# Kernel optimization log

Measured on AMD Instinct MI355X. Metric: run time of the kernel, lower is better.

Reference implementation:

```python
import jax, jax.numpy as jnp
import numpy as np
import math

D = 512          # model_dim
H = 8            # num_heads
HD = D // H      # head_dim
L = 6            # num_layers
FF = 2 * D       # dim_feedforward
IN_DIM = 24
MAX_LEN = 1024   # positional_embedding_dim (sinusoidal max_len)
NUM_CLASSES = 1
B, S = 8, 1024
EPS = 1e-5


def make_sinusoidal_pe(max_len, d_model):
    position = np.arange(max_len, dtype=np.float32)[:, None]
    div_term = np.exp(np.arange(0, d_model, 2, dtype=np.float32) * (-math.log(10000.0) / d_model))
    pe = np.zeros((max_len, d_model), dtype=np.float32)
    pe[:, 0::2] = np.sin(position * div_term)
    pe[:, 1::2] = np.cos(position * div_term)
    return jnp.asarray(pe)


def layer_norm(x, g, b):
    mu = jnp.mean(x, axis=-1, keepdims=True)
    var = jnp.mean(jnp.square(x - mu), axis=-1, keepdims=True)
    return (x - mu) * jax.lax.rsqrt(var + EPS) * g + b


def setup_inputs() -> dict:
    key = jax.random.key(0)
    ks = jax.random.split(key, 16)
    xavier = lambda k, shape: jax.random.uniform(
        k, shape, jnp.float32,
        -math.sqrt(6.0 / (shape[-2] + shape[-1])),
        math.sqrt(6.0 / (shape[-2] + shape[-1])))
    inp = {
        'x': jax.random.normal(ks[0], (B, S, IN_DIM), jnp.float32),
        'positions': jax.random.randint(ks[1], (B, S), 0, MAX_LEN),
        'pe': make_sinusoidal_pe(MAX_LEN, D),
        'input_W': xavier(ks[2], (IN_DIM, D)),
        'input_b': jnp.zeros((D,), jnp.float32),
        'qkv_W': xavier(ks[3], (L, D, 3 * D)),
        'qkv_b': jnp.zeros((L, 3 * D), jnp.float32),
        'o_W': xavier(ks[4], (L, D, D)),
        'o_b': jnp.zeros((L, D), jnp.float32),
        'ff1_W': xavier(ks[5], (L, D, FF)),
        'ff1_b': jnp.zeros((L, FF), jnp.float32),
        'ff2_W': xavier(ks[6], (L, FF, D)),
        'ff2_b': jnp.zeros((L, D), jnp.float32),
        'ln1_g': jnp.ones((L, D), jnp.float32),
        'ln1_b': jnp.zeros((L, D), jnp.float32),
        'ln2_g': jnp.ones((L, D), jnp.float32),
        'ln2_b': jnp.zeros((L, D), jnp.float32),
        'out1_W': xavier(ks[7], (D, D)),
        'out1_b': jnp.zeros((D,), jnp.float32),
        'outln_g': jnp.ones((D,), jnp.float32),
        'outln_b': jnp.zeros((D,), jnp.float32),
        'out2_W': xavier(ks[8], (D, NUM_CLASSES)),
        'out2_b': jnp.zeros((NUM_CLASSES,), jnp.float32),
    }
    return inp


def reference(x, positions, pe, input_W, input_b, qkv_W, qkv_b, o_W, o_b,
              ff1_W, ff1_b, ff2_W, ff2_b, ln1_g, ln1_b, ln2_g, ln2_b,
              out1_W, out1_b, outln_g, outln_b, out2_W, out2_b):
    b, s, _ = x.shape
    # input projection + sinusoidal positional encoding gathered at positions
    h = x @ input_W + input_b + pe[positions]            # [B,S,D]
    scale = 1.0 / math.sqrt(HD)
    for l in range(qkv_W.shape[0]):
        qkv = (h @ qkv_W[l] + qkv_b[l]).reshape(b, s, H, 3 * HD)
        q = jnp.transpose(qkv[..., :HD], (0, 2, 1, 3))           # [B,H,S,hd]
        k = jnp.transpose(qkv[..., HD:2 * HD], (0, 2, 1, 3))
        v = jnp.transpose(qkv[..., 2 * HD:], (0, 2, 1, 3))
        logits = jnp.einsum('bhqd,bhkd->bhqk', q, k) * scale     # [B,H,S,S]
        attn = jax.nn.softmax(logits, axis=-1)
        vals = jnp.einsum('bhqk,bhkd->bhqd', attn, v)
        vals = jnp.transpose(vals, (0, 2, 1, 3)).reshape(b, s, D)
        attn_out = vals @ o_W[l] + o_b[l]
        h = layer_norm(h + attn_out, ln1_g[l], ln1_b[l])
        ff = jax.nn.relu(h @ ff1_W[l] + ff1_b[l]) @ ff2_W[l] + ff2_b[l]
        h = layer_norm(h + ff, ln2_g[l], ln2_b[l])
    pooled = jnp.mean(h, axis=1)                                 # [B,D] mean pooling
    o = jax.nn.relu(layer_norm(pooled @ out1_W + out1_b, outln_g, outln_b))
    return o @ out2_W + out2_b                                   # [B,num_classes]
```

## Files before the change

kernel.cpp:

```cpp
#include <hip/hip_runtime.h>
#include <cstddef>

#define EPS 1e-5f

typedef short bf16x8 __attribute__((ext_vector_type(8)));
typedef float f32x4 __attribute__((ext_vector_type(4)));
typedef unsigned short u16x8 __attribute__((ext_vector_type(8)));
typedef unsigned short u16x4 __attribute__((ext_vector_type(4)));

__device__ __forceinline__ unsigned short f2bf(float x) {
  unsigned u = __float_as_uint(x);
  return (unsigned short)((u + 0x7FFFu + ((u >> 16) & 1u)) >> 16);
}

__device__ __forceinline__ void gl2lds16(const unsigned short* g, unsigned short* l) {
  __builtin_amdgcn_global_load_lds(
      (const __attribute__((address_space(1))) unsigned int*)g,
      (__attribute__((address_space(3))) unsigned int*)l, 16, 0, 0);
}

__global__ __launch_bounds__(512) void inproj_kernel(
    const float* __restrict__ x, const int* __restrict__ pos,
    const float* __restrict__ pe, const float* __restrict__ Wp,
    const float* __restrict__ bp, float* __restrict__ h,
    unsigned short* __restrict__ hb) {
  int t = blockIdx.x, d = threadIdx.x;
  __shared__ float xs[24];
  if (d < 24) xs[d] = x[(size_t)t * 24 + d];
  __syncthreads();
  float acc = bp[d] + pe[(size_t)pos[t] * 512 + d];
#pragma unroll
  for (int k = 0; k < 24; ++k) acc += xs[k] * Wp[k * 512 + d];
  h[(size_t)t * 512 + d] = acc;
  hb[(size_t)t * 512 + d] = f2bf(acc);
}

__global__ __launch_bounds__(256) void wcast_kernel(
    const float* __restrict__ qw, const float* __restrict__ ow,
    const float* __restrict__ f1w, const float* __restrict__ f2w,
    unsigned short* __restrict__ qd, unsigned short* __restrict__ od,
    unsigned short* __restrict__ f1d, unsigned short* __restrict__ f2d) {
  __shared__ float sm[64][65];
  int bid = blockIdx.x;
  const float* src; unsigned short* dst; int K, N, tile;
  if (bid < 192)      { src = qw;  dst = qd;  K = 512;  N = 1536; tile = bid; }
  else if (bid < 256) { src = ow;  dst = od;  K = 512;  N = 512;  tile = bid - 192; }
  else if (bid < 384) { src = f1w; dst = f1d; K = 512;  N = 1024; tile = bid - 256; }
  else                { src = f2w; dst = f2d; K = 1024; N = 512;  tile = bid - 384; }
  int nt = N >> 6;
  int tk = tile / nt, tn = tile % nt;
  int k0 = tk * 64, n0 = tn * 64;
  int tid = threadIdx.x;
#pragma unroll
  for (int it = 0; it < 16; ++it) {
    int idx = it * 256 + tid;
    int ki = idx >> 6, ni = idx & 63;
    sm[ki][ni] = src[(size_t)(k0 + ki) * N + n0 + ni];
  }
  __syncthreads();
#pragma unroll
  for (int it = 0; it < 16; ++it) {
    int idx = it * 256 + tid;
    int ni = idx >> 6, ki = idx & 63;
    dst[(size_t)(n0 + ni) * K + k0 + ki] = f2bf(sm[ki][ni]);
  }
}

template <int MODE>
__global__ __launch_bounds__(256) void gemm_bf16(
    const unsigned short* __restrict__ A, const unsigned short* __restrict__ Bw,
    const float* __restrict__ bias, float* __restrict__ Cf,
    unsigned short* __restrict__ Cb, unsigned short* __restrict__ q_out,
    unsigned short* __restrict__ k_out, unsigned short* __restrict__ v_out,
    int M, int N, int K) {
  __shared__ unsigned short As[128 * 32];
  __shared__ unsigned short Bs[128 * 32];
  int tid = threadIdx.x;
  int w = tid >> 6, l = tid & 63;
  int wm = w >> 1, wn = w & 1;
  int cl = l & 15, kg = l >> 4;
  int n0 = blockIdx.x * 128, m0 = blockIdx.y * 128;
  f32x4 acc[4][4];
#pragma unroll
  for (int i = 0; i < 4; ++i)
#pragma unroll
    for (int j = 0; j < 4; ++j) acc[i][j] = f32x4{0.f, 0.f, 0.f, 0.f};

  const unsigned short* Ap = A + (size_t)m0 * K;
  const unsigned short* Bp = Bw + (size_t)n0 * K;

  for (int k0 = 0; k0 < K; k0 += 32) {
    __syncthreads();
#pragma unroll
    for (int c = 0; c < 2; ++c) {
      int idx = c * 256 + tid;
      int r = idx >> 2, kq = idx & 3;
      gl2lds16(Ap + (size_t)r * K + k0 + kq * 8, &As[(c * 256 + w * 64) * 8]);
      gl2lds16(Bp + (size_t)r * K + k0 + kq * 8, &Bs[(c * 256 + w * 64) * 8]);
    }
    __syncthreads();
    bf16x8 af[4], bfr[4];
#pragma unroll
    for (int i = 0; i < 4; ++i) {
      af[i]  = *(const bf16x8*)&As[(wm * 64 + i * 16 + cl) * 32 + kg * 8];
      bfr[i] = *(const bf16x8*)&Bs[(wn * 64 + i * 16 + cl) * 32 + kg * 8];
    }
#pragma unroll
    for (int i = 0; i < 4; ++i)
#pragma unroll
      for (int j = 0; j < 4; ++j)
        acc[i][j] = __builtin_amdgcn_mfma_f32_16x16x32_bf16(af[i], bfr[j], acc[i][j], 0, 0, 0);
  }

  int rl = kg * 4;
#pragma unroll
  for (int i = 0; i < 4; ++i) {
    int mbase = m0 + wm * 64 + i * 16 + rl;
#pragma unroll
    for (int j = 0; j < 4; ++j) {
      int col = n0 + wn * 64 + j * 16 + cl;
      float bv = bias[col];
      if (MODE == 0) {
#pragma unroll
        for (int r = 0; r < 4; ++r)
          Cf[(size_t)(mbase + r) * N + col] = acc[i][j][r] + bv;
      } else if (MODE == 1) {
#pragma unroll
        for (int r = 0; r < 4; ++r)
          Cb[(size_t)(mbase + r) * N + col] = f2bf(fmaxf(acc[i][j][r] + bv, 0.f));
      } else {
        int hh = col / 192;
        int rem = col - hh * 192;
        int which = rem >> 6, d = rem & 63;
        int b = mbase >> 10, s = mbase & 1023;
        if (which == 2) {
          u16x4 pk;
#pragma unroll
          for (int r = 0; r < 4; ++r) pk[r] = f2bf(acc[i][j][r] + bv);
          *(u16x4*)&v_out[((size_t)((b * 8 + hh) * 64 + d)) * 1024 + s] = pk;
        } else {
          unsigned short* dst = (which == 0) ? q_out : k_out;
#pragma unroll
          for (int r = 0; r < 4; ++r)
            dst[(((size_t)(b * 8 + hh)) * 1024 + s + r) * 64 + d] = f2bf(acc[i][j][r] + bv);
        }
      }
    }
  }
}

__global__ __launch_bounds__(512) void attn_mfma(
    const unsigned short* __restrict__ qT, const unsigned short* __restrict__ kT,
    const unsigned short* __restrict__ vT, unsigned short* __restrict__ valsb) {
  __shared__ unsigned short Ks[2][64 * 64];
  __shared__ unsigned short Vs[2][64 * 64];
  __shared__ unsigned short Ps[8][16 * 64];

  int bh = blockIdx.x >> 3;
  int qt = blockIdx.x & 7;
  int b = bh >> 3, h = bh & 7;
  int tid = threadIdx.x;
  int w = tid >> 6, l = tid & 63;
  int cl = l & 15, kg = l >> 4, rl = kg * 4;

  const unsigned short* kgb = kT + (size_t)bh * 65536;
  const unsigned short* vgb = vT + (size_t)bh * 65536;

  int q0 = qt * 128 + w * 16;
  const unsigned short* qbase = qT + ((size_t)bh * 1024 + q0) * 64;
  bf16x8 aq[2];
  aq[0] = *(const bf16x8*)(qbase + cl * 64 + kg * 8);
  aq[1] = *(const bf16x8*)(qbase + cl * 64 + 32 + kg * 8);

  int sk = tid >> 3, sa = tid & 7;
  int kboff = (sk * 128 + sa * 16) ^ ((sk & 7) << 4);

  const float C = 0.125f * 1.44269504f;

  float m2[4], lsum[4];
  f32x4 accO[4];
#pragma unroll
  for (int r = 0; r < 4; ++r) { m2[r] = -1e30f; lsum[r] = 0.f; }
#pragma unroll
  for (int df = 0; df < 4; ++df) accO[df] = f32x4{0.f, 0.f, 0.f, 0.f};

  char* Pw = (char*)&Ps[w][0];

  uint4 kv = *(const uint4*)(kgb + (size_t)sk * 64 + sa * 8);
  uint4 vv = *(const uint4*)(vgb + (size_t)sk * 1024 + sa * 8);
  *(uint4*)((char*)Ks[0] + kboff) = kv;
  *(uint4*)((char*)Vs[0] + kboff) = vv;
  __syncthreads();

  for (int c = 0; c < 16; ++c) {
    int cur = c & 1;
    if (c < 15) {
      kv = *(const uint4*)(kgb + (size_t)(c + 1) * 4096 + sk * 64 + sa * 8);
      vv = *(const uint4*)(vgb + (size_t)sk * 1024 + (c + 1) * 64 + sa * 8);
    }

    f32x4 s[4];
#pragma unroll
    for (int kf = 0; kf < 4; ++kf) {
      s[kf] = f32x4{0.f, 0.f, 0.f, 0.f};
#pragma unroll
      for (int ks = 0; ks < 2; ++ks) {
        int row = kf * 16 + cl;
        int boff = (row * 128 + ks * 64 + kg * 16) ^ ((row & 7) << 4);
        bf16x8 bk = *(const bf16x8*)((char*)Ks[cur] + boff);
        s[kf] = __builtin_amdgcn_mfma_f32_16x16x32_bf16(aq[ks], bk, s[kf], 0, 0, 0);
      }
    }

    float cm[4];
#pragma unroll
    for (int r = 0; r < 4; ++r)
      cm[r] = fmaxf(fmaxf(s[0][r], s[1][r]), fmaxf(s[2][r], s[3][r]));
#pragma unroll
    for (int off = 1; off < 16; off <<= 1)
#pragma unroll
      for (int r = 0; r < 4; ++r) cm[r] = fmaxf(cm[r], __shfl_xor(cm[r], off));

    float alpha[4];
#pragma unroll
    for (int r = 0; r < 4; ++r) {
      float mn = fmaxf(m2[r], cm[r] * C);
      alpha[r] = exp2f(m2[r] - mn);
      m2[r] = mn;
    }

    float rs[4] = {0.f, 0.f, 0.f, 0.f};
#pragma unroll
    for (int kf = 0; kf < 4; ++kf)
#pragma unroll
      for (int r = 0; r < 4; ++r) {
        float p = exp2f(s[kf][r] * C - m2[r]);
        rs[r] += p;
        int row = rl + r;
        int boff = (row * 128 + (kf * 16 + cl) * 2) ^ ((row & 7) << 4);
        *(unsigned short*)(Pw + boff) = f2bf(p);
      }
#pragma unroll
    for (int off = 1; off < 16; off <<= 1)
#pragma unroll
      for (int r = 0; r < 4; ++r) rs[r] += __shfl_xor(rs[r], off);
#pragma unroll
    for (int r = 0; r < 4; ++r) lsum[r] = lsum[r] * alpha[r] + rs[r];
#pragma unroll
    for (int df = 0; df < 4; ++df)
#pragma unroll
      for (int r = 0; r < 4; ++r) accO[df][r] *= alpha[r];

#pragma unroll
    for (int ks = 0; ks < 2; ++ks) {
      int pboff = (cl * 128 + ks * 64 + kg * 16) ^ ((cl & 7) << 4);
      bf16x8 ap = *(const bf16x8*)(Pw + pboff);
#pragma unroll
      for (int df = 0; df < 4; ++df) {
        int d = df * 16 + cl;
        int vboff = (d * 128 + ks * 64 + kg * 16) ^ ((d & 7) << 4);
        bf16x8 bv = *(const bf16x8*)((char*)Vs[cur] + vboff);
        accO[df] = __builtin_amdgcn_mfma_f32_16x16x32_bf16(ap, bv, accO[df], 0, 0, 0);
      }
    }

    if (c < 15) {
      *(uint4*)((char*)Ks[cur ^ 1] + kboff) = kv;
      *(uint4*)((char*)Vs[cur ^ 1] + kboff) = vv;
    }
    __syncthreads();
  }

  float inv[4];
#pragma unroll
  for (int r = 0; r < 4; ++r) inv[r] = 1.f / lsum[r];
#pragma unroll
  for (int df = 0; df < 4; ++df)
#pragma unroll
    for (int r = 0; r < 4; ++r) {
      int q = q0 + rl + r;
      int d = df * 16 + cl;
      valsb[(((size_t)b * 1024) + q) * 512 + h * 64 + d] = f2bf(accO[df][r] * inv[r]);
    }
}

__global__ __launch_bounds__(256) void ln_residual(
    float* __restrict__ h, const float* __restrict__ res,
    const float* __restrict__ g, const float* __restrict__ bb,
    unsigned short* __restrict__ hb) {
  int row = blockIdx.x * 4 + (threadIdx.x >> 6);
  int lane = threadIdx.x & 63;
  size_t base = (size_t)row * 512 + lane * 8;
  float4 v0 = *(const float4*)&h[base];
  float4 v1 = *(const float4*)&h[base + 4];
  float4 r0 = *(const float4*)&res[base];
  float4 r1 = *(const float4*)&res[base + 4];
  float xv[8];
  xv[0] = v0.x + r0.x; xv[1] = v0.y + r0.y; xv[2] = v0.z + r0.z; xv[3] = v0.w + r0.w;
  xv[4] = v1.x + r1.x; xv[5] = v1.y + r1.y; xv[6] = v1.z + r1.z; xv[7] = v1.w + r1.w;
  float s = 0.f, sq = 0.f;
#pragma unroll
  for (int i = 0; i < 8; ++i) { s += xv[i]; sq += xv[i] * xv[i]; }
#pragma unroll
  for (int off = 32; off; off >>= 1) { s += __shfl_xor(s, off); sq += __shfl_xor(sq, off); }
  float mu = s * (1.f / 512.f);
  float var = sq * (1.f / 512.f) - mu * mu;
  float rstd = rsqrtf(var + EPS);
  float4 g0 = *(const float4*)&g[lane * 8];
  float4 g1 = *(const float4*)&g[lane * 8 + 4];
  float4 b0 = *(const float4*)&bb[lane * 8];
  float4 b1 = *(const float4*)&bb[lane * 8 + 4];
  float o[8];
  o[0] = (xv[0] - mu) * rstd * g0.x + b0.x;
  o[1] = (xv[1] - mu) * rstd * g0.y + b0.y;
  o[2] = (xv[2] - mu) * rstd * g0.z + b0.z;
  o[3] = (xv[3] - mu) * rstd * g0.w + b0.w;
  o[4] = (xv[4] - mu) * rstd * g1.x + b1.x;
  o[5] = (xv[5] - mu) * rstd * g1.y + b1.y;
  o[6] = (xv[6] - mu) * rstd * g1.z + b1.z;
  o[7] = (xv[7] - mu) * rstd * g1.w + b1.w;
  *(float4*)&h[base] = make_float4(o[0], o[1], o[2], o[3]);
  *(float4*)&h[base + 4] = make_float4(o[4], o[5], o[6], o[7]);
  u16x8 hv;
#pragma unroll
  for (int i = 0; i < 8; ++i) hv[i] = f2bf(o[i]);
  *(u16x8*)&hb[base] = hv;
}

__global__ __launch_bounds__(512) void pool_kernel(
    const float* __restrict__ h, float* __restrict__ partial) {
  int b = blockIdx.x >> 3, c = blockIdx.x & 7, d = threadIdx.x;
  float s = 0.f;
  for (int t = 0; t < 128; ++t)
    s += h[((size_t)b * 1024 + c * 128 + t) * 512 + d];
  partial[(size_t)blockIdx.x * 512 + d] = s;
}

__global__ __launch_bounds__(512) void head_kernel(
    const float* __restrict__ partial, const float* __restrict__ W1,
    const float* __restrict__ b1, const float* __restrict__ g,
    const float* __restrict__ bb, const float* __restrict__ W2,
    const float* __restrict__ b2, float* __restrict__ out) {
  int b = blockIdx.x, tid = threadIdx.x;
  int wid = tid >> 6, lane = tid & 63;
  __shared__ float ps[512];
  __shared__ float red_s[8];
  __shared__ float red_q[8];
  float pv = 0.f;
#pragma unroll
  for (int c = 0; c < 8; ++c) pv += partial[((size_t)(b * 8 + c)) * 512 + tid];
  ps[tid] = pv * (1.f / 1024.f);
  __syncthreads();
  float acc = b1[tid];
  for (int k = 0; k < 512; ++k) acc += ps[k] * W1[(size_t)k * 512 + tid];
  float s = acc, sq = acc * acc;
#pragma unroll
  for (int off = 32; off; off >>= 1) { s += __shfl_xor(s, off); sq += __shfl_xor(sq, off); }
  if (lane == 0) { red_s[wid] = s; red_q[wid] = sq; }
  __syncthreads();
  float S = 0.f, Q = 0.f;
#pragma unroll
  for (int i = 0; i < 8; ++i) { S += red_s[i]; Q += red_q[i]; }
  float mu = S * (1.f / 512.f);
  float var = Q * (1.f / 512.f) - mu * mu;
  float rstd = rsqrtf(var + EPS);
  float z = (acc - mu) * rstd * g[tid] + bb[tid];
  float r = fmaxf(z, 0.f);
  float v = r * W2[tid];
#pragma unroll
  for (int off = 32; off; off >>= 1) v += __shfl_xor(v, off);
  __syncthreads();
  if (lane == 0) red_s[wid] = v;
  __syncthreads();
  if (tid == 0) {
    float t = 0.f;
#pragma unroll
    for (int i = 0; i < 8; ++i) t += red_s[i];
    out[b] = t + b2[0];
  }
}

extern "C" void kernel_launch(void* const* d_in, const int* in_sizes, int n_in,
                              void* d_out, int out_size, void* d_ws, size_t ws_size,
                              hipStream_t stream) {
  const float* x    = (const float*)d_in[0];
  const int*   pos  = (const int*)d_in[1];
  const float* pe   = (const float*)d_in[2];
  const float* inW  = (const float*)d_in[3];
  const float* inb  = (const float*)d_in[4];
  const float* qkvW = (const float*)d_in[5];
  const float* qkvb = (const float*)d_in[6];
  const float* oW   = (const float*)d_in[7];
  const float* ob   = (const float*)d_in[8];
  const float* f1W  = (const float*)d_in[9];
  const float* f1b  = (const float*)d_in[10];
  const float* f2W  = (const float*)d_in[11];
  const float* f2b  = (const float*)d_in[12];
  const float* l1g  = (const float*)d_in[13];
  const float* l1b  = (const float*)d_in[14];
  const float* l2g  = (const float*)d_in[15];
  const float* l2b  = (const float*)d_in[16];
  const float* o1W  = (const float*)d_in[17];
  const float* o1b  = (const float*)d_in[18];
  const float* og   = (const float*)d_in[19];
  const float* obb  = (const float*)d_in[20];
  const float* o2W  = (const float*)d_in[21];
  const float* o2b  = (const float*)d_in[22];
  float* out = (float*)d_out;

  char* W = (char*)d_ws;
  float*          h     = (float*)(W + 0);
  unsigned short* hb    = (unsigned short*)(W + 16777216);
  unsigned short* qTb   = (unsigned short*)(W + 25165824);
  unsigned short* kTb   = (unsigned short*)(W + 33554432);
  unsigned short* vTb   = (unsigned short*)(W + 41943040);
  unsigned short* valsb = (unsigned short*)(W + 50331648);
  float*          projf = (float*)(W + 25165824);
  unsigned short* ff1b  = (unsigned short*)(W + 41943040);
  unsigned short* wt    = (unsigned short*)(W + 58720256);
  float*          part  = (float*)(W + 62914560);

  unsigned short* wt_qkv = wt;
  unsigned short* wt_o   = wt + 786432;
  unsigned short* wt_f1  = wt + 1048576;
  unsigned short* wt_f2  = wt + 1572864;

  inproj_kernel<<<8192, 512, 0, stream>>>(x, pos, pe, inW, inb, h, hb);

  for (int l = 0; l < 6; ++l) {
    wcast_kernel<<<512, 256, 0, stream>>>(
        qkvW + (size_t)l * 512 * 1536, oW + (size_t)l * 512 * 512,
        f1W + (size_t)l * 512 * 1024, f2W + (size_t)l * 1024 * 512,
        wt_qkv, wt_o, wt_f1, wt_f2);

    gemm_bf16<2><<<dim3(12, 64), 256, 0, stream>>>(
        hb, wt_qkv, qkvb + l * 1536, nullptr, nullptr, qTb, kTb, vTb,
        8192, 1536, 512);

    attn_mfma<<<512, 512, 0, stream>>>(qTb, kTb, vTb, valsb);

    gemm_bf16<0><<<dim3(4, 64), 256, 0, stream>>>(
        valsb, wt_o, ob + l * 512, projf, nullptr, nullptr, nullptr, nullptr,
        8192, 512, 512);

    ln_residual<<<2048, 256, 0, stream>>>(h, projf, l1g + l * 512, l1b + l * 512, hb);

    gemm_bf16<1><<<dim3(8, 64), 256, 0, stream>>>(
        hb, wt_f1, f1b + l * 1024, nullptr, ff1b, nullptr, nullptr, nullptr,
        8192, 1024, 512);

    gemm_bf16<0><<<dim3(4, 64), 256, 0, stream>>>(
        ff1b, wt_f2, f2b + l * 512, projf, nullptr, nullptr, nullptr, nullptr,
        8192, 512, 1024);

    ln_residual<<<2048, 256, 0, stream>>>(h, projf, l2g + l * 512, l2b + l * 512, hb);
  }

  pool_kernel<<<64, 512, 0, stream>>>(h, part);
  head_kernel<<<8, 512, 0, stream>>>(part, o1W, o1b, og, obb, o2W, o2b, out);
}
```

Baseline: 1.221 ms.

## Widen GEMM K-tile with swizzled LDS and restructure attention with lazy rescaling

The GEMM now stages 64-wide K tiles with an XOR-swizzled LDS layout, halving the number of barrier-separated iterations and reducing bank conflicts. The attention kernel processes 128-key chunks in single-buffered LDS with register prefetch. It also skips the online-softmax max update and rescale unless some row's max grows by more than a threshold, and defers the row-sum shuffle reduction to the end. This cuts per-chunk shuffles, exp work and barriers, at the cost of more LDS per block, possible occupancy loss, and the loss of double buffering in attention.

```diff
diff --git a/kernel.cpp b/kernel.cpp
--- a/kernel.cpp
+++ b/kernel.cpp
@@ -73,8 +73,8 @@
     unsigned short* __restrict__ Cb, unsigned short* __restrict__ q_out,
     unsigned short* __restrict__ k_out, unsigned short* __restrict__ v_out,
     int M, int N, int K) {
-  __shared__ unsigned short As[128 * 32];
-  __shared__ unsigned short Bs[128 * 32];
+  __shared__ unsigned short As[128 * 64];
+  __shared__ unsigned short Bs[128 * 64];
   int tid = threadIdx.x;
   int w = tid >> 6, l = tid & 63;
   int wm = w >> 1, wn = w & 1;
@@ -89,27 +89,42 @@
   const unsigned short* Ap = A + (size_t)m0 * K;
   const unsigned short* Bp = Bw + (size_t)n0 * K;
 
-  for (int k0 = 0; k0 < K; k0 += 32) {
+  for (int k0 = 0; k0 < K; k0 += 64) {
     __syncthreads();
 #pragma unroll
-    for (int c = 0; c < 2; ++c) {
+    for (int c = 0; c < 4; ++c) {
       int idx = c * 256 + tid;
-      int r = idx >> 2, kq = idx & 3;
+      int r = idx >> 3;
+      int kq = (idx & 7) ^ (r & 7);
       gl2lds16(Ap + (size_t)r * K + k0 + kq * 8, &As[(c * 256 + w * 64) * 8]);
+    }
+#pragma unroll
+    for (int c = 0; c < 4; ++c) {
+      int idx = c * 256 + tid;
+      int r = idx >> 3;
+      int kq = (idx & 7) ^ (r & 7);
       gl2lds16(Bp + (size_t)r * K + k0 + kq * 8, &Bs[(c * 256 + w * 64) * 8]);
     }
     __syncthreads();
-    bf16x8 af[4], bfr[4];
+    bf16x8 af[4][2], bfr[4][2];
+    int key = (cl & 7) << 4;
 #pragma unroll
     for (int i = 0; i < 4; ++i) {
-      af[i]  = *(const bf16x8*)&As[(wm * 64 + i * 16 + cl) * 32 + kg * 8];
-      bfr[i] = *(const bf16x8*)&Bs[(wn * 64 + i * 16 + cl) * 32 + kg * 8];
+      int rowa = wm * 64 + i * 16 + cl;
+      int rowb = wn * 64 + i * 16 + cl;
+#pragma unroll
+      for (int s2 = 0; s2 < 2; ++s2) {
+        af[i][s2]  = *(const bf16x8*)((char*)As + ((rowa * 128 + s2 * 64 + kg * 16) ^ key));
+        bfr[i][s2] = *(const bf16x8*)((char*)Bs + ((rowb * 128 + s2 * 64 + kg * 16) ^ key));
+      }
     }
 #pragma unroll
     for (int i = 0; i < 4; ++i)
 #pragma unroll
-      for (int j = 0; j < 4; ++j)
-        acc[i][j] = __builtin_amdgcn_mfma_f32_16x16x32_bf16(af[i], bfr[j], acc[i][j], 0, 0, 0);
+      for (int j = 0; j < 4; ++j) {
+        acc[i][j] = __builtin_amdgcn_mfma_f32_16x16x32_bf16(af[i][0], bfr[j][0], acc[i][j], 0, 0, 0);
+        acc[i][j] = __builtin_amdgcn_mfma_f32_16x16x32_bf16(af[i][1], bfr[j][1], acc[i][j], 0, 0, 0);
+      }
   }
 
   int rl = kg * 4;
@@ -152,9 +167,9 @@
 __global__ __launch_bounds__(512) void attn_mfma(
     const unsigned short* __restrict__ qT, const unsigned short* __restrict__ kT,
     const unsigned short* __restrict__ vT, unsigned short* __restrict__ valsb) {
-  __shared__ unsigned short Ks[2][64 * 64];
-  __shared__ unsigned short Vs[2][64 * 64];
-  __shared__ unsigned short Ps[8][16 * 64];
+  __shared__ unsigned short Ks[128 * 64];
+  __shared__ unsigned short Vs[64 * 128];
+  __shared__ unsigned short Ps[8][16 * 128];
 
   int bh = blockIdx.x >> 3;
   int qt = blockIdx.x & 7;
@@ -172,11 +187,14 @@
   aq[0] = *(const bf16x8*)(qbase + cl * 64 + kg * 8);
   aq[1] = *(const bf16x8*)(qbase + cl * 64 + 32 + kg * 8);
 
-  int sk = tid >> 3, sa = tid & 7;
-  int kboff = (sk * 128 + sa * 16) ^ ((sk & 7) << 4);
+  int kk = tid >> 3, ka = tid & 7;
+  int vd = tid >> 4, vs = tid & 15;
+  int kb0 = (kk * 128 + ka * 16) ^ ((kk & 7) << 4);
+  int kb1 = kb0 + 64 * 128;
+  int vb0 = (vd * 256 + vs * 16) ^ ((vd & 7) << 4);
+  int vb1 = vb0 + 32 * 256;
 
   const float C = 0.125f * 1.44269504f;
-
   float m2[4], lsum[4];
   f32x4 accO[4];
 #pragma unroll
@@ -186,90 +204,98 @@
 
   char* Pw = (char*)&Ps[w][0];
 
-  uint4 kv = *(const uint4*)(kgb + (size_t)sk * 64 + sa * 8);
-  uint4 vv = *(const uint4*)(vgb + (size_t)sk * 1024 + sa * 8);
-  *(uint4*)((char*)Ks[0] + kboff) = kv;
-  *(uint4*)((char*)Vs[0] + kboff) = vv;
-  __syncthreads();
-
-  for (int c = 0; c < 16; ++c) {
-    int cur = c & 1;
-    if (c < 15) {
-      kv = *(const uint4*)(kgb + (size_t)(c + 1) * 4096 + sk * 64 + sa * 8);
-      vv = *(const uint4*)(vgb + (size_t)sk * 1024 + (c + 1) * 64 + sa * 8);
-    }
-
-    f32x4 s[4];
-#pragma unroll
-    for (int kf = 0; kf < 4; ++kf) {
+  uint4 kr0 = *(const uint4*)(kgb + (size_t)kk * 64 + ka * 8);
+  uint4 kr1 = *(const uint4*)(kgb + (size_t)(kk + 64) * 64 + ka * 8);
+  uint4 vr0 = *(const uint4*)(vgb + (size_t)vd * 1024 + vs * 8);
+  uint4 vr1 = *(const uint4*)(vgb + (size_t)(vd + 32) * 1024 + vs * 8);
+
+  for (int c = 0; c < 8; ++c) {
+    __syncthreads();
+    *(uint4*)((char*)Ks + kb0) = kr0;
+    *(uint4*)((char*)Ks + kb1) = kr1;
+    *(uint4*)((char*)Vs + vb0) = vr0;
+    *(uint4*)((char*)Vs + vb1) = vr1;
+    if (c < 7) {
+      kr0 = *(const uint4*)(kgb + (size_t)((c + 1) * 128 + kk) * 64 + ka * 8);
+      kr1 = *(const uint4*)(kgb + (size_t)((c + 1) * 128 + kk + 64) * 64 + ka * 8);
+      vr0 = *(const uint4*)(vgb + (size_t)vd * 1024 + (c + 1) * 128 + vs * 8);
+      vr1 = *(const uint4*)(vgb + (size_t)(vd + 32) * 1024 + (c + 1) * 128 + vs * 8);
+    }
+    __syncthreads();
+
+    f32x4 s[8];
+    int keyq = (cl & 7) << 4;
+#pragma unroll
+    for (int kf = 0; kf < 8; ++kf) {
       s[kf] = f32x4{0.f, 0.f, 0.f, 0.f};
+      int row = kf * 16 + cl;
 #pragma unroll
       for (int ks = 0; ks < 2; ++ks) {
-        int row = kf * 16 + cl;
-        int boff = (row * 128 + ks * 64 + kg * 16) ^ ((row & 7) << 4);
-        bf16x8 bk = *(const bf16x8*)((char*)Ks[cur] + boff);
-        s[kf] = __builtin_amdgcn_mfma_f32_16x16x32_bf16(aq[ks], bk, s[kf], 0, 0, 0);
-      }
-    }
-
-    float cm[4];
-#pragma unroll
-    for (int r = 0; r < 4; ++r)
-      cm[r] = fmaxf(fmaxf(s[0][r], s[1][r]), fmaxf(s[2][r], s[3][r]));
-#pragma unroll
-    for (int off = 1; off < 16; off <<= 1)
-#pragma unroll
-      for (int r = 0; r < 4; ++r) cm[r] = fmaxf(cm[r], __shfl_xor(cm[r], off));
-
-    float alpha[4];
+        int boff = (row * 128 + ks * 64 + kg * 16) ^ keyq;
+        s[kf] = __builtin_amdgcn_mfma_f32_16x16x32_bf16(
+            aq[ks], *(const bf16x8*)((char*)Ks + boff), s[kf], 0, 0, 0);
+      }
+    }
+
+    float lmax[4];
 #pragma unroll
     for (int r = 0; r < 4; ++r) {
-      float mn = fmaxf(m2[r], cm[r] * C);
-      alpha[r] = exp2f(m2[r] - mn);
-      m2[r] = mn;
-    }
-
-    float rs[4] = {0.f, 0.f, 0.f, 0.f};
-#pragma unroll
-    for (int kf = 0; kf < 4; ++kf)
+      float a0 = fmaxf(fmaxf(s[0][r], s[1][r]), fmaxf(s[2][r], s[3][r]));
+      float a1 = fmaxf(fmaxf(s[4][r], s[5][r]), fmaxf(s[6][r], s[7][r]));
+      lmax[r] = fmaxf(a0, a1);
+    }
+    float need = fmaxf(fmaxf(lmax[0] * C - m2[0], lmax[1] * C - m2[1]),
+                       fmaxf(lmax[2] * C - m2[2], lmax[3] * C - m2[3]));
+    if (!__all(need <= 8.0f)) {
+      float cm[4];
+#pragma unroll
+      for (int r = 0; r < 4; ++r) cm[r] = lmax[r];
+#pragma unroll
+      for (int off = 1; off < 16; off <<= 1)
+#pragma unroll
+        for (int r = 0; r < 4; ++r) cm[r] = fmaxf(cm[r], __shfl_xor(cm[r], off));
+#pragma unroll
+      for (int r = 0; r < 4; ++r) {
+        float mn = fmaxf(m2[r], cm[r] * C);
+        float alpha = exp2f(m2[r] - mn);
+        m2[r] = mn;
+        lsum[r] *= alpha;
+        accO[0][r] *= alpha; accO[1][r] *= alpha;
+        accO[2][r] *= alpha; accO[3][r] *= alpha;
+      }
+    }
+
+#pragma unroll
+    for (int kf = 0; kf < 8; ++kf) {
 #pragma unroll
       for (int r = 0; r < 4; ++r) {
         float p = exp2f(s[kf][r] * C - m2[r]);
-        rs[r] += p;
+        lsum[r] += p;
         int row = rl + r;
-        int boff = (row * 128 + (kf * 16 + cl) * 2) ^ ((row & 7) << 4);
-        *(unsigned short*)(Pw + boff) = f2bf(p);
-      }
-#pragma unroll
-    for (int off = 1; off < 16; off <<= 1)
-#pragma unroll
-      for (int r = 0; r < 4; ++r) rs[r] += __shfl_xor(rs[r], off);
-#pragma unroll
-    for (int r = 0; r < 4; ++r) lsum[r] = lsum[r] * alpha[r] + rs[r];
-#pragma unroll
-    for (int df = 0; df < 4; ++df)
-#pragma unroll
-      for (int r = 0; r < 4; ++r) accO[df][r] *= alpha[r];
-
-#pragma unroll
-    for (int ks = 0; ks < 2; ++ks) {
-      int pboff = (cl * 128 + ks * 64 + kg * 16) ^ ((cl & 7) << 4);
+        int boff = (row * 256 + (kf * 16 + cl) * 2) ^ ((row & 7) << 4);
+        *(unsigned short*)(Pw + boff) =
+            (unsigned short)((__float_as_uint(p) + 0x8000u) >> 16);
+      }
+    }
+
+#pragma unroll
+    for (int ks = 0; ks < 4; ++ks) {
+      int pboff = (cl * 256 + ks * 64 + kg * 16) ^ ((cl & 7) << 4);
       bf16x8 ap = *(const bf16x8*)(Pw + pboff);
 #pragma unroll
       for (int df = 0; df < 4; ++df) {
         int d = df * 16 + cl;
-        int vboff = (d * 128 + ks * 64 + kg * 16) ^ ((d & 7) << 4);
-        bf16x8 bv = *(const bf16x8*)((char*)Vs[cur] + vboff);
-        accO[df] = __builtin_amdgcn_mfma_f32_16x16x32_bf16(ap, bv, accO[df], 0, 0, 0);
-      }
-    }
-
-    if (c < 15) {
-      *(uint4*)((char*)Ks[cur ^ 1] + kboff) = kv;
-      *(uint4*)((char*)Vs[cur ^ 1] + kboff) = vv;
-    }
-    __syncthreads();
-  }
+        int vboff = (d * 256 + ks * 64 + kg * 16) ^ ((d & 7) << 4);
+        accO[df] = __builtin_amdgcn_mfma_f32_16x16x32_bf16(
+            ap, *(const bf16x8*)((char*)Vs + vboff), accO[df], 0, 0, 0);
+      }
+    }
+  }
+
+#pragma unroll
+  for (int off = 1; off < 16; off <<= 1)
+#pragma unroll
+    for (int r = 0; r < 4; ++r) lsum[r] += __shfl_xor(lsum[r], off);
 
   float inv[4];
 #pragma unroll
```

After: 1.156 ms. 1.06x faster.
